# Kernel optimization log

Measured on AMD Instinct MI355X. Metric: run time of the kernel, lower is better.

Reference implementation:

```python
import jax, jax.numpy as jnp
import numpy as np

N_ENTITIES = 100000
N_EDGES = 1250000
N_RELATIONS = 32
D = 64


def setup_inputs() -> dict:
    key = jax.random.key(0)
    k1, k2, k3, k4 = jax.random.split(key, 4)
    entity_emb = jax.random.normal(k1, (N_ENTITIES, D), dtype=jnp.float32)
    edge_index = jax.random.randint(k2, (2, N_EDGES), 0, N_ENTITIES, dtype=jnp.int64)
    edge_type = jax.random.randint(k3, (N_EDGES,), 0, N_RELATIONS, dtype=jnp.int64)
    weight = jax.random.normal(k4, (N_RELATIONS, D), dtype=jnp.float32)
    return {"entity_emb": entity_emb, "edge_index": edge_index,
            "edge_type": edge_type, "weight": weight}


def reference(entity_emb, edge_index, edge_type, weight):
    n_entities = entity_emb.shape[0]
    head, tail = edge_index[0], edge_index[1]
    # gather tail entity embeddings and relation embeddings, elementwise multiply
    neigh_relation_emb = entity_emb[tail] * weight[edge_type]  # [E, D]
    # scatter_mean by head index
    sums = jax.ops.segment_sum(neigh_relation_emb, head, num_segments=n_entities)
    counts = jax.ops.segment_sum(jnp.ones((head.shape[0],), dtype=entity_emb.dtype),
                                 head, num_segments=n_entities)
    entity_agg = sums / jnp.maximum(counts, 1.0)[:, None]  # empty segments -> 0
    return entity_agg
```

## Files before the change

### kernel.cpp

```cpp
#include <hip/hip_runtime.h>

#define D 64
#define BIN_SHIFT 7
#define BIN_SIZE 128
#define MAX_BINS 1024
#define BINCAP 2560
#define K1_THREADS 1024
#define K1_EPT 5
#define K1_EPB (K1_THREADS * K1_EPT)
#define K2_THREADS 512
#define NREL 32


__device__ __forceinline__ float bf2f(unsigned short u) {
    union { unsigned i; float f; } x; x.i = ((unsigned)u) << 16; return x.f;
}

__global__ void __launch_bounds__(K1_THREADS)
prep_kernel(const float* __restrict__ emb,
            unsigned short* __restrict__ emb16,
            const int* __restrict__ head,
            const int* __restrict__ tail,
            const int* __restrict__ etype,
            int* __restrict__ binCount,
            unsigned* __restrict__ recs,
            int nbins, int n_edges, long n4, int nsort) {
    __shared__ unsigned srec[K1_EPB];
    __shared__ int hist[MAX_BINS];
    __shared__ int base[MAX_BINS + 1];
    __shared__ int cur[MAX_BINS];
    __shared__ int gpos[MAX_BINS];
    __shared__ unsigned short binof[K1_EPB];
    __shared__ int wtot[16];
    __shared__ int wexcl[16];

    int tid = threadIdx.x;

    if (blockIdx.x >= nsort) {
        long i = (long)(blockIdx.x - nsort) * K1_THREADS + tid;
        if (i >= n4) return;
        float4 v = ((const float4*)emb)[i];
        ushort4 o;
        unsigned b;
        b = __float_as_uint(v.x); o.x = (unsigned short)((b + 0x7FFF + ((b >> 16) & 1)) >> 16);
        b = __float_as_uint(v.y); o.y = (unsigned short)((b + 0x7FFF + ((b >> 16) & 1)) >> 16);
        b = __float_as_uint(v.z); o.z = (unsigned short)((b + 0x7FFF + ((b >> 16) & 1)) >> 16);
        b = __float_as_uint(v.w); o.w = (unsigned short)((b + 0x7FFF + ((b >> 16) & 1)) >> 16);
        ((ushort4*)emb16)[i] = o;
        return;
    }

    hist[tid] = 0;
    __syncthreads();

    long blockBase = (long)blockIdx.x * K1_EPB;
    int nvalid = (int)(((long)n_edges - blockBase < (long)K1_EPB)
                       ? ((long)n_edges - blockBase) : (long)K1_EPB);

    unsigned rv[K1_EPT]; int bv[K1_EPT];
#pragma unroll
    for (int k = 0; k < K1_EPT; k++) {
        long e = blockBase + (long)k * K1_THREADS + tid;
        if (e < n_edges) {
            int h = head[e];
            bv[k] = h >> BIN_SHIFT;
            rv[k] = (unsigned)tail[e] | ((unsigned)etype[e] << 17)
                  | ((unsigned)(h & (BIN_SIZE - 1)) << 22);
            atomicAdd(&hist[bv[k]], 1);
        } else bv[k] = -1;
    }
    __syncthreads();

    int lane = tid & 63, wv = tid >> 6;
    int h0 = hist[tid];
    int v = h0;
#pragma unroll
    for (int s = 1; s < 64; s <<= 1) {
        int x = __shfl_up(v, s);
        if (lane >= s) v += x;
    }
    if (lane == 63) wtot[wv] = v;
    __syncthreads();
    if (wv == 0 && lane < 16) {
        int t = wtot[lane];
        int a = t;
#pragma unroll
        for (int s = 1; s < 16; s <<= 1) {
            int x = __shfl_up(a, s);
            if (lane >= s) a += x;
        }
        wexcl[lane] = a - t;
    }
    __syncthreads();
    int incl = v + wexcl[wv];
    base[tid] = incl - h0;  cur[tid] = incl - h0;
    if (tid == K1_THREADS - 1) base[MAX_BINS] = incl;
    __syncthreads();

    if (tid < nbins) {
        int c = hist[tid];
        gpos[tid] = (c > 0) ? atomicAdd(&binCount[tid], c) : 0;
    }
    __syncthreads();

#pragma unroll
    for (int k = 0; k < K1_EPT; k++) {
        if (bv[k] >= 0) {
            int p = atomicAdd(&cur[bv[k]], 1);
            srec[p] = rv[k];
        }
    }
    __syncthreads();

    if (tid < nbins) {
        int j0 = base[tid], j1 = base[tid + 1];
        for (int j = j0; j < j1; j++) binof[j] = (unsigned short)tid;
    }
    __syncthreads();

    for (int i = tid; i < nvalid; i += K1_THREADS) {
        int b = binof[i];
        int off = gpos[b] + (i - base[b]);
        if (off < BINCAP)
            recs[(long)b * BINCAP + off] = srec[i];
    }
}

__global__ void __launch_bounds__(K2_THREADS, 2)
aggregate_bin_kernel(const unsigned short* __restrict__ emb16,
                     const float* __restrict__ weight,
                     const unsigned* __restrict__ recs,
                     const int* __restrict__ binCount,
                     float* __restrict__ out, int n_ent) {
    __shared__ unsigned raw[BINCAP];
    __shared__ unsigned sorted[BINCAP + 16];
    __shared__ float wlds[NREL * D];
    __shared__ float wz[D];
    __shared__ int hist[BIN_SIZE];
    __shared__ int off[BIN_SIZE];
    __shared__ int cur[BIN_SIZE];

    int tid = threadIdx.x;
    int b = blockIdx.x;
    int n = min(binCount[b], BINCAP);

    if (tid < 16) sorted[n + tid] = 0u;
    if (tid >= 448 && tid < 448 + D) wz[tid - 448] = 0.f;
    for (int i = tid; i < NREL * D; i += K2_THREADS) wlds[i] = weight[i];
    if (tid < BIN_SIZE) hist[tid] = 0;
    __syncthreads();

    const unsigned* gr = recs + (long)b * BINCAP;
    for (int i = tid; i < n; i += K2_THREADS) {
        unsigned q = gr[i];
        raw[i] = q;
        atomicAdd(&hist[(q >> 22) & 127], 1);
    }
    __syncthreads();

    int lane = tid & 63;
    int wave = tid >> 6;

    if (wave == 0) {
        int h0 = hist[lane];
        int h1 = hist[64 + lane];
        int s0 = h0, s1 = h1;
#pragma unroll
        for (int s = 1; s < 64; s <<= 1) {
            int t0 = __shfl_up(s0, s);
            int t1 = __shfl_up(s1, s);
            if (lane >= s) { s0 += t0; s1 += t1; }
        }
        int tot0 = __shfl(s0, 63);
        int e0 = s0 - h0;
        int e1 = tot0 + s1 - h1;
        off[lane] = e0;      cur[lane] = e0;
        off[64 + lane] = e1; cur[64 + lane] = e1;
    }
    __syncthreads();

    for (int i = tid; i < n; i += K2_THREADS) {
        unsigned q = raw[i];
        int p = atomicAdd(&cur[(q >> 22) & 127], 1);
        sorted[p] = q;
    }
    __syncthreads();

    int g = lane >> 4;
    int c4 = (lane & 15) << 2;
    int hbase = b << BIN_SHIFT;

    int oA, dA, oB, dB;
    unsigned qa0, qa1, qa2, qa3, qb0, qb1, qb2, qb3;
    ushort4 ua0, ua1, ua2, ua3, ub0, ub1, ub2, ub3;
    float4 wa0, wa1, wa2, wa3, wb0, wb1, wb2, wb3;

#define K2_PREF(J, o_, d_, q0, q1, q2, q3, u0, u1, u2, u3, w0, w1, w2, w3)    \
    do {                                                                       \
        int hh_ = wave + ((J) << 3);                                           \
        o_ = off[hh_]; d_ = hist[hh_];                                         \
        q0 = sorted[o_ + g];      q1 = sorted[o_ + 4 + g];                     \
        q2 = sorted[o_ + 8 + g];  q3 = sorted[o_ + 12 + g];                    \
        bool k0 = (g < d_), k1 = (4 + g < d_), k2 = (8 + g < d_),              \
             k3 = (12 + g < d_);                                               \
        q0 = k0 ? q0 : 0u;  q1 = k1 ? q1 : 0u;                                 \
        q2 = k2 ? q2 : 0u;  q3 = k3 ? q3 : 0u;                                 \
        u0 = *(const ushort4*)&emb16[((long)(q0 & 0x1FFFF) << 6) + c4];        \
        u1 = *(const ushort4*)&emb16[((long)(q1 & 0x1FFFF) << 6) + c4];        \
        u2 = *(const ushort4*)&emb16[((long)(q2 & 0x1FFFF) << 6) + c4];        \
        u3 = *(const ushort4*)&emb16[((long)(q3 & 0x1FFFF) << 6) + c4];        \
        w0 = *(const float4*)(k0 ? &wlds[(((q0 >> 17) & 31) << 6) + c4]        \
                                 : &wz[c4]);                                   \
        w1 = *(const float4*)(k1 ? &wlds[(((q1 >> 17) & 31) << 6) + c4]        \
                                 : &wz[c4]);                                   \
        w2 = *(const float4*)(k2 ? &wlds[(((q2 >> 17) & 31) << 6) + c4]        \
                                 : &wz[c4]);                                   \
        w3 = *(const float4*)(k3 ? &wlds[(((q3 >> 17) & 31) << 6) + c4]        \
                                 : &wz[c4]);                                   \
    } while (0)

#define K2_COMP(J, o_, d_, q0, q1, q2, q3, u0, u1, u2, u3, w0, w1, w2, w3)    \
    do {                                                                       \
        int hh_ = wave + ((J) << 3);                                           \
        float4 acc = make_float4(0.f, 0.f, 0.f, 0.f);                          \
        acc.x += bf2f(u0.x) * w0.x; acc.y += bf2f(u0.y) * w0.y;                \
        acc.z += bf2f(u0.z) * w0.z; acc.w += bf2f(u0.w) * w0.w;                \
        acc.x += bf2f(u1.x) * w1.x; acc.y += bf2f(u1.y) * w1.y;                \
        acc.z += bf2f(u1.z) * w1.z; acc.w += bf2f(u1.w) * w1.w;                \
        acc.x += bf2f(u2.x) * w2.x; acc.y += bf2f(u2.y) * w2.y;                \
        acc.z += bf2f(u2.z) * w2.z; acc.w += bf2f(u2.w) * w2.w;                \
        acc.x += bf2f(u3.x) * w3.x; acc.y += bf2f(u3.y) * w3.y;                \
        acc.z += bf2f(u3.z) * w3.z; acc.w += bf2f(u3.w) * w3.w;                \
        for (int i_ = 16; i_ < d_; i_ += 16) {          \
            int e0_ = i_ + g, e1_ = i_ + 4 + g, e2_ = i_ + 8 + g,              \
                e3_ = i_ + 12 + g;                                             \
            unsigned t0 = sorted[o_ + e0_]; unsigned t1 = sorted[o_ + e1_];    \
            unsigned t2 = sorted[o_ + e2_]; unsigned t3 = sorted[o_ + e3_];    \
            bool c0 = (e0_ < d_), c1 = (e1_ < d_), c2 = (e2_ < d_),            \
                 c3 = (e3_ < d_);                                              \
            t0 = c0 ? t0 : 0u;  t1 = c1 ? t1 : 0u;                             \
            t2 = c2 ? t2 : 0u;  t3 = c3 ? t3 : 0u;                             \
            ushort4 v0 = *(const ushort4*)&emb16[((long)(t0 & 0x1FFFF) << 6) + c4]; \
            ushort4 v1 = *(const ushort4*)&emb16[((long)(t1 & 0x1FFFF) << 6) + c4]; \
            ushort4 v2 = *(const ushort4*)&emb16[((long)(t2 & 0x1FFFF) << 6) + c4]; \
            ushort4 v3 = *(const ushort4*)&emb16[((long)(t3 & 0x1FFFF) << 6) + c4]; \
            float4 x0 = *(const float4*)(c0 ? &wlds[(((t0 >> 17) & 31) << 6) + c4] \
                                            : &wz[c4]);                        \
            float4 x1 = *(const float4*)(c1 ? &wlds[(((t1 >> 17) & 31) << 6) + c4] \
                                            : &wz[c4]);                        \
            float4 x2 = *(const float4*)(c2 ? &wlds[(((t2 >> 17) & 31) << 6) + c4] \
                                            : &wz[c4]);                        \
            float4 x3 = *(const float4*)(c3 ? &wlds[(((t3 >> 17) & 31) << 6) + c4] \
                                            : &wz[c4]);                        \
            acc.x += bf2f(v0.x) * x0.x; acc.y += bf2f(v0.y) * x0.y;            \
            acc.z += bf2f(v0.z) * x0.z; acc.w += bf2f(v0.w) * x0.w;            \
            acc.x += bf2f(v1.x) * x1.x; acc.y += bf2f(v1.y) * x1.y;            \
            acc.z += bf2f(v1.z) * x1.z; acc.w += bf2f(v1.w) * x1.w;            \
            acc.x += bf2f(v2.x) * x2.x; acc.y += bf2f(v2.y) * x2.y;            \
            acc.z += bf2f(v2.z) * x2.z; acc.w += bf2f(v2.w) * x2.w;            \
            acc.x += bf2f(v3.x) * x3.x; acc.y += bf2f(v3.y) * x3.y;            \
            acc.z += bf2f(v3.z) * x3.z; acc.w += bf2f(v3.w) * x3.w;            \
        }                                                                      \
        acc.x += __shfl_xor(acc.x, 16); acc.y += __shfl_xor(acc.y, 16);        \
        acc.z += __shfl_xor(acc.z, 16); acc.w += __shfl_xor(acc.w, 16);        \
        acc.x += __shfl_xor(acc.x, 32); acc.y += __shfl_xor(acc.y, 32);        \
        acc.z += __shfl_xor(acc.z, 32); acc.w += __shfl_xor(acc.w, 32);        \
        if (g == 0 && hbase + hh_ < n_ent) {                                   \
            float inv = 1.f / fmaxf((float)d_, 1.f);                           \
            *(float4*)&out[((long)(hbase + hh_) << 6) + c4] =                  \
                make_float4(acc.x * inv, acc.y * inv, acc.z * inv, acc.w * inv);\
        }                                                                      \
    } while (0)

    K2_PREF(0, oA, dA, qa0, qa1, qa2, qa3, ua0, ua1, ua2, ua3, wa0, wa1, wa2, wa3);
#pragma unroll 1
    for (int j = 0; j < 16; j += 2) {
        K2_PREF(j + 1, oB, dB, qb0, qb1, qb2, qb3, ub0, ub1, ub2, ub3,
                wb0, wb1, wb2, wb3);
        K2_COMP(j, oA, dA, qa0, qa1, qa2, qa3, ua0, ua1, ua2, ua3,
                wa0, wa1, wa2, wa3);
        int jn = (j + 2 < 16) ? (j + 2) : 15;
        K2_PREF(jn, oA, dA, qa0, qa1, qa2, qa3, ua0, ua1, ua2, ua3,
                wa0, wa1, wa2, wa3);
        K2_COMP(j + 1, oB, dB, qb0, qb1, qb2, qb3, ub0, ub1, ub2, ub3,
                wb0, wb1, wb2, wb3);
    }
#undef K2_PREF
#undef K2_COMP
}

__global__ void fb_scatter(const float* __restrict__ emb, const int* __restrict__ head,
                           const int* __restrict__ tail, const int* __restrict__ etype,
                           const float* __restrict__ weight, float* __restrict__ out,
                           float* __restrict__ cnt, int n_edges) {
    int gtid = blockIdx.x * blockDim.x + threadIdx.x;
    int e = gtid >> 6, lane = threadIdx.x & 63;
    if (e >= n_edges) return;
    int h = head[e], t = tail[e], r = etype[e];
    atomicAdd(&out[(long)h * D + lane], emb[(long)t * D + lane] * weight[r * D + lane]);
    if (lane == 0) atomicAdd(&cnt[h], 1.0f);
}
__global__ void fb_divide(float* __restrict__ out, const float* __restrict__ cnt, int n) {
    int i = blockIdx.x * blockDim.x + threadIdx.x;
    if (i < n) out[i] = out[i] / fmaxf(cnt[i >> 6], 1.0f);
}


extern "C" void kernel_launch(void* const* d_in, const int* in_sizes, int n_in,
                              void* d_out, int out_size, void* d_ws, size_t ws_size,
                              hipStream_t stream) {
    const float* emb    = (const float*)d_in[0];
    const int*   eidx   = (const int*)  d_in[1];
    const int*   etype  = (const int*)  d_in[2];
    const float* weight = (const float*)d_in[3];
    float* out = (float*)d_out;

    int n_edges = in_sizes[2];
    int n_ent   = out_size / D;
    const int* head = eidx;
    const int* tail = eidx + n_edges;

    int nbins = (n_ent + BIN_SIZE - 1) >> BIN_SHIFT;
    size_t recs_bytes = sizeof(int) * ((size_t)nbins * BINCAP);
    size_t cnt_bytes  = sizeof(int) * (size_t)nbins;
    size_t emb16_off  = (cnt_bytes + recs_bytes + 15) & ~((size_t)15);
    size_t need = emb16_off + (size_t)n_ent * D * sizeof(unsigned short);
    long mean_load = (n_ent > 0) ? ((long)n_edges * BIN_SIZE / n_ent) : 0;
    bool ok = (n_ent <= 131072) && (nbins <= MAX_BINS) && (ws_size >= need) &&
              (mean_load + 700 <= BINCAP);

    if (ok) {
        int* binCount  = (int*)d_ws;
        unsigned* recs = (unsigned*)(binCount + nbins);
        unsigned short* emb16 = (unsigned short*)((char*)d_ws + emb16_off);

        long n4 = (long)n_ent * D / 4;
        int nsort = (n_edges + K1_EPB - 1) / K1_EPB;
        int ncvt  = (int)((n4 + K1_THREADS - 1) / K1_THREADS);

        hipMemsetAsync(binCount, 0, (size_t)nbins * sizeof(int), stream);
        prep_kernel<<<nsort + ncvt, K1_THREADS, 0, stream>>>(
            emb, emb16, head, tail, etype, binCount, recs,
            nbins, n_edges, n4, nsort);

        aggregate_bin_kernel<<<nbins, K2_THREADS, 0, stream>>>(
            emb16, weight, recs, binCount, out, n_ent);
    } else {
        float* cnt = (float*)d_ws;
        hipMemsetAsync(out, 0, (size_t)out_size * sizeof(float), stream);
        hipMemsetAsync(cnt, 0, (size_t)n_ent * sizeof(float), stream);
        long tt = (long)n_edges * 64;
        fb_scatter<<<(int)((tt + 255) / 256), 256, 0, stream>>>(
            emb, head, tail, etype, weight, out, cnt, n_edges);
        fb_divide<<<(out_size + 255) / 256, 256, 0, stream>>>(out, cnt, out_size);
    }
}
```

Before: 146.1 us.

## Stage gathered embedding rows into LDS via async global_load_lds double buffering

Replaces the register-based software prefetch of bf16 embedding rows with direct global-to-LDS async loads (global_load_lds, 16 bytes per lane) into per-wave double-buffered slots. The raw staging buffer is enlarged and reused as the per-wave slots, and an explicit s_waitcnt vmcnt(2) gates each compute step. The goal is to cut register pressure and keep more gather traffic in flight. In exchange it adds LDS footprint, which can lower occupancy, and it relies on manual waitcnt handling, which is fragile. Without a barrier there is also a risk of reading LDS before the data is visible, or of overwriting raw while other waves are still using it.

```diff
diff --git a/kernel.cpp b/kernel.cpp
--- a/kernel.cpp
+++ b/kernel.cpp
@@ -11,6 +11,9 @@
 #define K2_THREADS 512
 #define NREL 32
 
+
+typedef __attribute__((address_space(3))) unsigned char lds_u8_t;
+typedef __attribute__((address_space(1))) const unsigned char gbl_u8_t;
 
 __device__ __forceinline__ float bf2f(unsigned short u) {
     union { unsigned i; float f; } x; x.i = ((unsigned)u) << 16; return x.f;
@@ -132,13 +135,15 @@
                      const unsigned* __restrict__ recs,
                      const int* __restrict__ binCount,
                      float* __restrict__ out, int n_ent) {
-    __shared__ unsigned raw[BINCAP];
+    __shared__ unsigned stage_raw[8192];
     __shared__ unsigned sorted[BINCAP + 16];
     __shared__ float wlds[NREL * D];
     __shared__ float wz[D];
     __shared__ int hist[BIN_SIZE];
     __shared__ int off[BIN_SIZE];
     __shared__ int cur[BIN_SIZE];
+
+    unsigned* raw = stage_raw;
 
     int tid = threadIdx.x;
     int b = blockIdx.x;
@@ -188,41 +193,52 @@
 
     int g = lane >> 4;
     int c4 = (lane & 15) << 2;
+    int r8 = lane >> 3;
+    int ch8 = lane & 7;
     int hbase = b << BIN_SHIFT;
-
-    int oA, dA, oB, dB;
-    unsigned qa0, qa1, qa2, qa3, qb0, qb1, qb2, qb3;
-    ushort4 ua0, ua1, ua2, ua3, ub0, ub1, ub2, ub3;
-    float4 wa0, wa1, wa2, wa3, wb0, wb1, wb2, wb3;
-
-#define K2_PREF(J, o_, d_, q0, q1, q2, q3, u0, u1, u2, u3, w0, w1, w2, w3)    \
+    char* mySlot = (char*)stage_raw + wave * 4096;
+
+#define K2_STAGE(J, SLOT)                                                      \
     do {                                                                       \
         int hh_ = wave + ((J) << 3);                                           \
-        o_ = off[hh_]; d_ = hist[hh_];                                         \
-        q0 = sorted[o_ + g];      q1 = sorted[o_ + 4 + g];                     \
-        q2 = sorted[o_ + 8 + g];  q3 = sorted[o_ + 12 + g];                    \
-        bool k0 = (g < d_), k1 = (4 + g < d_), k2 = (8 + g < d_),              \
-             k3 = (12 + g < d_);                                               \
-        q0 = k0 ? q0 : 0u;  q1 = k1 ? q1 : 0u;                                 \
-        q2 = k2 ? q2 : 0u;  q3 = k3 ? q3 : 0u;                                 \
-        u0 = *(const ushort4*)&emb16[((long)(q0 & 0x1FFFF) << 6) + c4];        \
-        u1 = *(const ushort4*)&emb16[((long)(q1 & 0x1FFFF) << 6) + c4];        \
-        u2 = *(const ushort4*)&emb16[((long)(q2 & 0x1FFFF) << 6) + c4];        \
-        u3 = *(const ushort4*)&emb16[((long)(q3 & 0x1FFFF) << 6) + c4];        \
-        w0 = *(const float4*)(k0 ? &wlds[(((q0 >> 17) & 31) << 6) + c4]        \
-                                 : &wz[c4]);                                   \
-        w1 = *(const float4*)(k1 ? &wlds[(((q1 >> 17) & 31) << 6) + c4]        \
-                                 : &wz[c4]);                                   \
-        w2 = *(const float4*)(k2 ? &wlds[(((q2 >> 17) & 31) << 6) + c4]        \
-                                 : &wz[c4]);                                   \
-        w3 = *(const float4*)(k3 ? &wlds[(((q3 >> 17) & 31) << 6) + c4]        \
-                                 : &wz[c4]);                                   \
+        int o_ = off[hh_], d_ = hist[hh_];                                     \
+        int ea_ = r8, eb_ = 8 + r8;                                            \
+        unsigned qa_ = (ea_ < d_) ? sorted[o_ + ea_] : 0u;                     \
+        unsigned qb_ = (eb_ < d_) ? sorted[o_ + eb_] : 0u;                     \
+        const unsigned short* ga_ =                                            \
+            &emb16[((long)(qa_ & 0x1FFFF) << 6) + (ch8 << 3)];                 \
+        const unsigned short* gb_ =                                            \
+            &emb16[((long)(qb_ & 0x1FFFF) << 6) + (ch8 << 3)];                 \
+        char* l0_ = mySlot + (SLOT) * 2048;                                    \
+        __builtin_amdgcn_global_load_lds((gbl_u8_t*)ga_, (lds_u8_t*)l0_,       \
+                                         16, 0, 0);                            \
+        __builtin_amdgcn_global_load_lds((gbl_u8_t*)gb_,                       \
+                                         (lds_u8_t*)(l0_ + 1024), 16, 0, 0);   \
     } while (0)
 
-#define K2_COMP(J, o_, d_, q0, q1, q2, q3, u0, u1, u2, u3, w0, w1, w2, w3)    \
+#define K2_COMP(J, SLOT)                                                       \
     do {                                                                       \
         int hh_ = wave + ((J) << 3);                                           \
+        int o_ = off[hh_], d_ = hist[hh_];                                     \
+        const unsigned short* S_ =                                             \
+            (const unsigned short*)(mySlot + (SLOT) * 2048);                   \
         float4 acc = make_float4(0.f, 0.f, 0.f, 0.f);                          \
+        int e0 = g, e1 = 4 + g, e2 = 8 + g, e3 = 12 + g;                       \
+        unsigned q0 = sorted[o_ + e0]; unsigned q1 = sorted[o_ + e1];          \
+        unsigned q2 = sorted[o_ + e2]; unsigned q3 = sorted[o_ + e3];          \
+        bool k0 = (e0 < d_), k1 = (e1 < d_), k2 = (e2 < d_), k3 = (e3 < d_);   \
+        ushort4 u0 = *(const ushort4*)&S_[(e0 << 6) + c4];                     \
+        ushort4 u1 = *(const ushort4*)&S_[(e1 << 6) + c4];                     \
+        ushort4 u2 = *(const ushort4*)&S_[(e2 << 6) + c4];                     \
+        ushort4 u3 = *(const ushort4*)&S_[(e3 << 6) + c4];                     \
+        float4 w0 = *(const float4*)(k0 ? &wlds[(((q0 >> 17) & 31) << 6) + c4] \
+                                        : &wz[c4]);                            \
+        float4 w1 = *(const float4*)(k1 ? &wlds[(((q1 >> 17) & 31) << 6) + c4] \
+                                        : &wz[c4]);                            \
+        float4 w2 = *(const float4*)(k2 ? &wlds[(((q2 >> 17) & 31) << 6) + c4] \
+                                        : &wz[c4]);                            \
+        float4 w3 = *(const float4*)(k3 ? &wlds[(((q3 >> 17) & 31) << 6) + c4] \
+                                        : &wz[c4]);                            \
         acc.x += bf2f(u0.x) * w0.x; acc.y += bf2f(u0.y) * w0.y;                \
         acc.z += bf2f(u0.z) * w0.z; acc.w += bf2f(u0.w) * w0.w;                \
         acc.x += bf2f(u1.x) * w1.x; acc.y += bf2f(u1.y) * w1.y;                \
@@ -231,7 +247,7 @@
         acc.z += bf2f(u2.z) * w2.z; acc.w += bf2f(u2.w) * w2.w;                \
         acc.x += bf2f(u3.x) * w3.x; acc.y += bf2f(u3.y) * w3.y;                \
         acc.z += bf2f(u3.z) * w3.z; acc.w += bf2f(u3.w) * w3.w;                \
-        for (int i_ = 16; i_ < d_; i_ += 16) {          \
+        for (int i_ = 16; i_ < d_; i_ += 16) {   \
             int e0_ = i_ + g, e1_ = i_ + 4 + g, e2_ = i_ + 8 + g,              \
                 e3_ = i_ + 12 + g;                                             \
             unsigned t0 = sorted[o_ + e0_]; unsigned t1 = sorted[o_ + e1_];    \
@@ -272,20 +288,15 @@
         }                                                                      \
     } while (0)
 
-    K2_PREF(0, oA, dA, qa0, qa1, qa2, qa3, ua0, ua1, ua2, ua3, wa0, wa1, wa2, wa3);
+    K2_STAGE(0, 0);
+    K2_STAGE(1, 1);
 #pragma unroll 1
-    for (int j = 0; j < 16; j += 2) {
-        K2_PREF(j + 1, oB, dB, qb0, qb1, qb2, qb3, ub0, ub1, ub2, ub3,
-                wb0, wb1, wb2, wb3);
-        K2_COMP(j, oA, dA, qa0, qa1, qa2, qa3, ua0, ua1, ua2, ua3,
-                wa0, wa1, wa2, wa3);
-        int jn = (j + 2 < 16) ? (j + 2) : 15;
-        K2_PREF(jn, oA, dA, qa0, qa1, qa2, qa3, ua0, ua1, ua2, ua3,
-                wa0, wa1, wa2, wa3);
-        K2_COMP(j + 1, oB, dB, qb0, qb1, qb2, qb3, ub0, ub1, ub2, ub3,
-                wb0, wb1, wb2, wb3);
-    }
-#undef K2_PREF
+    for (int j = 0; j < 16; ++j) {
+        asm volatile("s_waitcnt vmcnt(2)" ::: "memory");
+        K2_COMP(j, j & 1);
+        if (j < 14) K2_STAGE(j + 2, j & 1);
+    }
+#undef K2_STAGE
 #undef K2_COMP
 }
 
```

New measurement: 154.3 us. +5.7%, slower.
